# Optimization experiments

Measured on AMD Instinct MI355X. Metric: run time of the kernel, lower is better.

## Reference

```python
import jax, jax.numpy as jnp
import numpy as np

N = 20000      # total nodes (100 graphs x 200 nodes)
B = 100        # batch_size
PER = 200      # nodes per graph (uniform) -> max_num_nodes
E = 320000     # edges (before self-loops)
F_IN = 32      # num_features
HEADS = 10
OUT = 128      # output_dim
NEG_SLOPE = 0.2  # PyG GATConv default


def setup_inputs() -> dict:
    key = jax.random.key(0)
    ks = jax.random.split(key, 14)
    feats = jax.random.normal(ks[0], (N, F_IN), jnp.float32)
    src = jax.random.randint(ks[1], (E,), 0, N)
    dst = jax.random.randint(ks[2], (E,), 0, N)
    edge_index = jnp.stack([src, dst]).astype(jnp.int32)
    graph_id = jnp.repeat(jnp.arange(B, dtype=jnp.int32), PER)
    batch_num_nodes = jnp.full((B,), PER, jnp.int32)
    s1 = 1.0 / np.sqrt(F_IN)
    s2 = 1.0 / np.sqrt(F_IN * HEADS)
    s3 = 1.0 / np.sqrt(OUT)
    return {
        "feats": feats,
        "edge_index": edge_index,
        "graph_id": graph_id,
        "batch_num_nodes": batch_num_nodes,
        # GATConv 1: in F_IN -> HEADS x F_IN, concat
        "W1": jax.random.normal(ks[3], (F_IN, HEADS * F_IN), jnp.float32) * s1,
        "a1_src": jax.random.normal(ks[4], (HEADS, F_IN), jnp.float32) * s1,
        "a1_dst": jax.random.normal(ks[5], (HEADS, F_IN), jnp.float32) * s1,
        "b1": jnp.zeros((HEADS * F_IN,), jnp.float32),
        "W2": jax.random.normal(ks[6], (HEADS * F_IN, OUT), jnp.float32) * s2,
        "a2_src": jax.random.normal(ks[7], (1, OUT), jnp.float32) * s3,
        "a2_dst": jax.random.normal(ks[8], (1, OUT), jnp.float32) * s3,
        "b2": jnp.zeros((OUT,), jnp.float32),
        # shared fc_g1
        "fc_w": jax.random.normal(ks[9], (OUT, OUT), jnp.float32) * s3,
        "fc_b": jnp.zeros((OUT,), jnp.float32),
    }


def gat_conv(x, src, dst, W, a_src, a_dst, bias, heads, out_dim):
    # x: [N, Fin]; src/dst already include self-loops (PyG default add_self_loops=True)
    n = x.shape[0]
    xw = (x @ W).reshape(n, heads, out_dim)                 # [N,H,F]
    s_src = jnp.einsum('nhf,hf->nh', xw, a_src)             # [N,H]
    s_dst = jnp.einsum('nhf,hf->nh', xw, a_dst)
    e = jax.nn.leaky_relu(s_src[src] + s_dst[dst], NEG_SLOPE)  # [E,H]
    # segment softmax over incoming edges of each destination node
    m = jax.ops.segment_max(e, dst, num_segments=n)         # [N,H]
    ex = jnp.exp(e - m[dst])
    denom = jax.ops.segment_sum(ex, dst, num_segments=n)    # [N,H]
    alpha = ex / jnp.maximum(denom[dst], 1e-16)             # [E,H]
    out = jax.ops.segment_sum(alpha[:, :, None] * xw[src], dst, num_segments=n)  # [N,H,F]
    return out.reshape(n, heads * out_dim) + bias


def reference(feats, edge_index, graph_id, batch_num_nodes,
              W1, a1_src, a1_dst, b1, W2, a2_src, a2_dst, b2, fc_w, fc_b):
    n = feats.shape[0]
    loops = jnp.arange(n, dtype=edge_index.dtype)
    src = jnp.concatenate([edge_index[0], loops])
    dst = jnp.concatenate([edge_index[1], loops])
    x = feats.astype(jnp.float32)
    # dropout layers are identity in eval mode
    x = jax.nn.elu(gat_conv(x, src, dst, W1, a1_src, a1_dst, b1, HEADS, F_IN))
    x = gat_conv(x, src, dst, W2, a2_src, a2_dst, b2, 1, OUT)
    x = jax.nn.relu(x)                                       # [N, OUT]
    # dgl_split: scatter node feats into [B, max_num_nodes, OUT] padded tensor
    cum = jnp.concatenate([jnp.zeros((1,), jnp.int32),
                           jnp.cumsum(batch_num_nodes).astype(jnp.int32)])
    idx = jnp.arange(n, dtype=jnp.int32) - cum[graph_id] + graph_id * PER
    padded = jnp.zeros((B * PER, OUT), x.dtype).at[idx].set(x).reshape(B, PER, OUT)
    out = jax.nn.relu(padded @ fc_w + fc_b)                  # [B, PER, OUT]
    # global max pool per graph, then shared fc_g1 + relu
    pooled = jax.ops.segment_max(x, graph_id, num_segments=B)  # [B, OUT]
    pooled = jax.nn.relu(pooled @ fc_w + fc_b)
    return (out, pooled)
```

## Files before the change

### kernel.cpp

```cpp
#include <hip/hip_runtime.h>

#define N_NODES 20000
#define N_EDGES 320000
#define ETOT    (N_EDGES + N_NODES)
#define HEADS   10
#define F_IN    32
#define C1      (HEADS * F_IN)
#define C2      128
#define NB      100
#define PER     200
#define CAP     96
#define HSTRIDE 328
#define X2STRIDE 136

typedef __attribute__((ext_vector_type(8))) short bf16x8;
typedef __attribute__((ext_vector_type(4))) float floatx4;
typedef _Float16 f16;
typedef _Float16 f16x2 __attribute__((ext_vector_type(2)));
typedef _Float16 f16x4 __attribute__((ext_vector_type(4)));
typedef _Float16 f16x8 __attribute__((ext_vector_type(8)));

static __device__ __forceinline__ unsigned short f2bf(float f) {
    unsigned int u = __float_as_uint(f);
    unsigned int r = (u + 0x7fffu + ((u >> 16) & 1u)) >> 16;
    return (unsigned short)r;
}

#define SCAT_BLOCKS  ((ETOT + 255) / 256)
#define SCORE_BLOCKS ((N_NODES + 63) / 64)
#define W2P_BLOCKS   ((C1 * C2 + 255) / 256)
#define W1P_BLOCKS   ((HEADS * F_IN * F_IN + 255) / 256)
#define FCP_BLOCKS   ((C2 * C2 + 255) / 256)
#define F16_BLOCKS   ((N_NODES * F_IN / 4 + 255) / 256)
__global__ __launch_bounds__(256) void mega_prep_kernel(
        const int* __restrict__ ei, int* __restrict__ cursor, int* __restrict__ csr_src,
        const float* __restrict__ feats, f16* __restrict__ feats16,
        const float* __restrict__ W1, unsigned short* __restrict__ W1p,
        const float* __restrict__ W2, unsigned short* __restrict__ W2p,
        const float* __restrict__ fcw, f16* __restrict__ FCp,
        const float* __restrict__ a1s, const float* __restrict__ a1d,
        float* __restrict__ s_src, float* __restrict__ s_dst) {
    unsigned int b = blockIdx.x;
    if (b < SCAT_BLOCKS) {
        int e = b * 256 + threadIdx.x;
        if (e >= ETOT) return;
        int s, d;
        if (e < N_EDGES) { s = ei[e]; d = ei[N_EDGES + e]; }
        else             { s = e - N_EDGES; d = s; }
        int pos = atomicAdd(&cursor[d], 1);
        csr_src[(size_t)d * CAP + pos] = s;
        return;
    }
    b -= SCAT_BLOCKS;
    if (b < SCORE_BLOCKS) {
        __shared__ __align__(16) float A[64 * F_IN];
        __shared__ float Ws[C1], Wd[C1];
        int t = threadIdx.x;
        for (int o = t; o < C1; o += 256) {
            int k = o & 31, h = o >> 5;
            float ss = 0.f, dd = 0.f;
#pragma unroll
            for (int f = 0; f < F_IN; f++) {
                float wv = W1[k * C1 + h * 32 + f];
                ss += wv * a1s[h * 32 + f];
                dd += wv * a1d[h * 32 + f];
            }
            Ws[k * HEADS + h] = ss;
            Wd[k * HEADS + h] = dd;
        }
        int n0 = b * 64;
        int nrows = min(64, N_NODES - n0);
        const float4* fs = (const float4*)(feats + (size_t)n0 * F_IN);
        float4* Af = (float4*)A;
        for (int i = t; i < nrows * 8; i += 256) Af[i] = fs[i];
        __syncthreads();
        for (int o = t; o < nrows * HEADS; o += 256) {
            int nl = o / HEADS, h = o - nl * HEADS;
            const float* ar = A + nl * F_IN;
            float ss = 0.f, dd = 0.f;
#pragma unroll
            for (int k = 0; k < F_IN; k++) {
                float av = ar[k];
                ss += av * Ws[k * HEADS + h];
                dd += av * Wd[k * HEADS + h];
            }
            s_src[(size_t)(n0 + nl) * HEADS + h] = ss;
            s_dst[(size_t)(n0 + nl) * HEADS + h] = dd;
        }
        return;
    }
    b -= SCORE_BLOCKS;
    if (b < W2P_BLOCKS) {
        int o = b * 256 + threadIdx.x;
        if (o >= C1 * C2) return;
        int j    = o & 7;
        int lane = (o >> 3) & 63;
        int ct   = (o >> 9) & 7;
        int kb   = o >> 12;
        int k = kb * 32 + (lane >> 4) * 8 + j;
        int n = ct * 16 + (lane & 15);
        W2p[o] = f2bf(W2[k * C2 + n]);
        return;
    }
    b -= W2P_BLOCKS;
    if (b < W1P_BLOCKS) {
        int o = b * 256 + threadIdx.x;
        if (o >= HEADS * F_IN * F_IN) return;
        int j    = o & 7;
        int lane = (o >> 3) & 63;
        int ct   = (o >> 9) & 1;
        int h    = o >> 10;
        int k = (lane >> 4) * 8 + j;
        int f = ct * 16 + (lane & 15);
        W1p[o] = f2bf(W1[k * C1 + h * 32 + f]);
        return;
    }
    b -= W1P_BLOCKS;
    if (b < FCP_BLOCKS) {
        int o = b * 256 + threadIdx.x;
        if (o >= C2 * C2) return;
        int j    = o & 7;
        int lane = (o >> 3) & 63;
        int ct   = (o >> 9) & 7;
        int kb   = o >> 12;
        int k = kb * 32 + (lane >> 4) * 8 + j;
        int n = ct * 16 + (lane & 15);
        FCp[o] = (f16)fcw[k * C2 + n];
        return;
    }
    b -= FCP_BLOCKS;
    {
        int o = b * 256 + threadIdx.x;
        if (o < N_NODES * F_IN / 4) {
            float4 v = ((const float4*)feats)[o];
            f16* d = feats16 + 4 * o;
            d[0] = (f16)v.x; d[1] = (f16)v.y; d[2] = (f16)v.z; d[3] = (f16)v.w;
        }
    }
}

__global__ __launch_bounds__(512) void agg1h1g2_kernel(
        const f16* __restrict__ feats16, const float* __restrict__ s_src,
        const float* __restrict__ s_dst, const int* __restrict__ deg_arr,
        const int* __restrict__ csr_src,
        const unsigned short* __restrict__ W1p, const float* __restrict__ b1,
        const unsigned short* __restrict__ W2p,
        const float* __restrict__ a_src, const float* __restrict__ a_dst,
        f16* __restrict__ xw2h, float* __restrict__ s_src2, float* __restrict__ s_dst2) {
    union Smem {
        struct { f16 P[16][HEADS * 32]; int S[16][32]; } p1;
        unsigned short H[16 * HSTRIDE];
    };
    __shared__ __align__(16) Smem u;
    __shared__ __align__(16) unsigned short G[16 * HSTRIDE];
    __shared__ float redS[8][16], redD[8][16];

    int tid   = threadIdx.x;
    int wslot = tid >> 6;
    int lane  = tid & 63;
    int r     = tid >> 5;
    int l     = tid & 31;
    int row0  = blockIdx.x * 16;
    f16* P = u.p1.P[r];
    int* S = u.p1.S[r];
    const f16x2 ones = {(f16)1.f, (f16)1.f};
    const char* fb = (const char*)feats16 + 2 * l;

    {
        int n = row0 + r;
        int beg = n * CAP, deg = deg_arr[n];
        const float* sdp = s_dst + (size_t)n * HEADS;
        float sd[10];
#pragma unroll
        for (int q = 0; q < 5; q++) {
            float2 v = *(const float2*)(sdp + 2 * q);
            sd[2 * q] = v.x; sd[2 * q + 1] = v.y;
        }
        float g[10], la[10];
#pragma unroll
        for (int h = 0; h < 10; h++) { g[h] = 0.f; la[h] = 0.f; }

        for (int c0 = 0; c0 < deg; c0 += 32) {
            int dc = min(deg - c0, 32);
            bool act = l < dc;
            int s_e = csr_src[beg + c0 + min(l, dc - 1)];
            const float* ssp = s_src + (size_t)s_e * HEADS;
            float p[10];
#pragma unroll
            for (int q = 0; q < 5; q++) {
                float2 v = *(const float2*)(ssp + 2 * q);
                float e0 = v.x + sd[2 * q];
                float e1 = v.y + sd[2 * q + 1];
                e0 = (e0 >= 0.f) ? e0 : 0.2f * e0;
                e1 = (e1 >= 0.f) ? e1 : 0.2f * e1;
                p[2 * q]     = act ? __expf(e0) : 0.f;
                p[2 * q + 1] = act ? __expf(e1) : 0.f;
            }
            S[l] = s_e << 6;
#pragma unroll
            for (int h = 0; h < 10; h++) P[h * 32 + l] = (f16)p[h];
            asm volatile("s_waitcnt lgkmcnt(0)" ::: "memory");

            int dcp = (dc + 1) & ~1;
            for (int i = 0; i < dcp; i += 2) {
                int2 ss2 = *(const int2*)&S[i];
                f16x2 v;
                v.x = *(const f16*)(fb + ss2.x);
                v.y = *(const f16*)(fb + ss2.y);
#pragma unroll
                for (int h = 0; h < 10; h++) {
                    f16x2 pp = *(const f16x2*)&P[h * 32 + i];
                    g[h]  = __builtin_amdgcn_fdot2(pp, v, g[h], false);
                    la[h] = __builtin_amdgcn_fdot2(pp, ones, la[h], false);
                }
            }
            asm volatile("s_waitcnt lgkmcnt(0)" ::: "memory");
        }
        unsigned short* gr = &G[r * HSTRIDE + l];
#pragma unroll
        for (int h = 0; h < 10; h++)
            gr[h * 32] = f2bf(g[h] / fmaxf(la[h], 1e-16f));
    }
    __syncthreads();

    int quad = lane >> 4, col = lane & 15;
    for (int h = wslot; h < 10; h += 8) {
        bf16x8 a = *(const bf16x8*)&G[col * HSTRIDE + h * 32 + quad * 8];
        bf16x8 bA = ((const bf16x8*)W1p)[(h * 2 + 0) * 64 + lane];
        bf16x8 bB = ((const bf16x8*)W1p)[(h * 2 + 1) * 64 + lane];
        floatx4 z = {0.f, 0.f, 0.f, 0.f};
        floatx4 c0 = __builtin_amdgcn_mfma_f32_16x16x32_bf16(a, bA, z, 0, 0, 0);
        floatx4 c1 = __builtin_amdgcn_mfma_f32_16x16x32_bf16(a, bB, z, 0, 0, 0);
        float bias0 = b1[h * 32 + col];
        float bias1 = b1[h * 32 + 16 + col];
#pragma unroll
        for (int reg = 0; reg < 4; reg++) {
            int rr = quad * 4 + reg;
            float o0 = c0[reg] + bias0;
            float o1 = c1[reg] + bias1;
            o0 = (o0 > 0.f) ? o0 : (__expf(o0) - 1.f);
            o1 = (o1 > 0.f) ? o1 : (__expf(o1) - 1.f);
            u.H[rr * HSTRIDE + h * 32 + col]      = f2bf(o0);
            u.H[rr * HSTRIDE + h * 32 + 16 + col] = f2bf(o1);
        }
    }
    __syncthreads();

    floatx4 acc = {0.f, 0.f, 0.f, 0.f};
    const bf16x8* pb = (const bf16x8*)W2p;
#pragma unroll
    for (int kb = 0; kb < 10; kb++) {
        bf16x8 a = *(const bf16x8*)&u.H[col * HSTRIDE + kb * 32 + quad * 8];
        bf16x8 b = pb[(kb * 8 + wslot) * 64 + lane];
        acc = __builtin_amdgcn_mfma_f32_16x16x32_bf16(a, b, acc, 0, 0, 0);
    }
    float asv = a_src[wslot * 16 + col];
    float adv = a_dst[wslot * 16 + col];
#pragma unroll
    for (int reg = 0; reg < 4; reg++) {
        int row = row0 + quad * 4 + reg;
        float v = acc[reg];
        xw2h[(size_t)row * C2 + wslot * 16 + col] = (f16)v;
        float vs = v * asv, vd = v * adv;
#pragma unroll
        for (int off = 8; off >= 1; off >>= 1) {
            vs += __shfl_xor(vs, off);
            vd += __shfl_xor(vd, off);
        }
        if (col == 0) { redS[wslot][quad * 4 + reg] = vs; redD[wslot][quad * 4 + reg] = vd; }
    }
    __syncthreads();
    if (wslot == 0) {
        if (lane < 16) {
            float s = 0.f;
#pragma unroll
            for (int w2 = 0; w2 < 8; w2++) s += redS[w2][lane];
            s_src2[row0 + lane] = s;
        } else if (lane < 32) {
            int r2 = lane - 16;
            float d = 0.f;
#pragma unroll
            for (int w2 = 0; w2 < 8; w2++) d += redD[w2][r2];
            s_dst2[row0 + r2] = d;
        }
    }
}

__global__ __launch_bounds__(512) void agg2fc_kernel(
        const f16* __restrict__ xw2h, const float* __restrict__ s_src2,
        const float* __restrict__ s_dst2, const int* __restrict__ deg_arr,
        const int* __restrict__ csr_src, const float* __restrict__ b2,
        const f16* __restrict__ FCp, const float* __restrict__ fcb,
        float* __restrict__ out, int* __restrict__ pooledi) {
    __shared__ __align__(8) int2 shE[16][32];
    __shared__ __align__(16) f16 X[16 * X2STRIDE];
    int tid   = threadIdx.x;
    int wslot = tid >> 6;
    int lane  = tid & 63;
    int r     = tid >> 5;
    int l     = tid & 31;
    int row0  = blockIdx.x * 16;
    int2* E = shE[r];
    const char* xb = (const char*)xw2h + 8 * l;

    {
        int n = row0 + r;
        int beg = n * CAP, deg = deg_arr[n];
        float sd = s_dst2[n];
        float ldn = 0.f, a0 = 0.f, a1 = 0.f, a2 = 0.f, a3 = 0.f;

        for (int c0 = 0; c0 < deg; c0 += 32) {
            int dc = min(deg - c0, 32);
            bool act = l < dc;
            int s_e = csr_src[beg + c0 + min(l, dc - 1)];
            float e = s_src2[s_e] + sd;
            e = (e >= 0.f) ? e : 0.2f * e;
            float p = act ? __expf(e) : 0.f;
            float su = p;
#pragma unroll
            for (int off = 16; off >= 1; off >>= 1) su += __shfl_xor(su, off);
            ldn += su;

            E[l] = make_int2(s_e << 8, __float_as_int(p));
            asm volatile("s_waitcnt lgkmcnt(0)" ::: "memory");

            int dcr = (dc + 3) & ~3;
            for (int i = 0; i < dcr; i += 4) {
                int2 e0 = E[i + 0], e1 = E[i + 1], e2 = E[i + 2], e3 = E[i + 3];
                f16x4 v0 = *(const f16x4*)(xb + e0.x);
                f16x4 v1 = *(const f16x4*)(xb + e1.x);
                f16x4 v2 = *(const f16x4*)(xb + e2.x);
                f16x4 v3 = *(const f16x4*)(xb + e3.x);
                float p0 = __int_as_float(e0.y), p1 = __int_as_float(e1.y);
                float p2 = __int_as_float(e2.y), p3 = __int_as_float(e3.y);
                a0 += p0 * (float)v0[0] + p1 * (float)v1[0] + p2 * (float)v2[0] + p3 * (float)v3[0];
                a1 += p0 * (float)v0[1] + p1 * (float)v1[1] + p2 * (float)v2[1] + p3 * (float)v3[1];
                a2 += p0 * (float)v0[2] + p1 * (float)v1[2] + p2 * (float)v2[2] + p3 * (float)v3[2];
                a3 += p0 * (float)v0[3] + p1 * (float)v1[3] + p2 * (float)v2[3] + p3 * (float)v3[3];
            }
            asm volatile("s_waitcnt lgkmcnt(0)" ::: "memory");
        }

        float linv = 1.f / fmaxf(ldn, 1e-16f);
        float4 bb = *(const float4*)(b2 + 4 * l);
        f16x4 o;
        o[0] = (f16)fmaxf(a0 * linv + bb.x, 0.f);
        o[1] = (f16)fmaxf(a1 * linv + bb.y, 0.f);
        o[2] = (f16)fmaxf(a2 * linv + bb.z, 0.f);
        o[3] = (f16)fmaxf(a3 * linv + bb.w, 0.f);
        *(f16x4*)&X[r * X2STRIDE + 4 * l] = o;
    }
    __syncthreads();

    int quad = lane >> 4, col = lane & 15;
    floatx4 acc = {0.f, 0.f, 0.f, 0.f};
    const f16x8* pb = (const f16x8*)FCp;
#pragma unroll
    for (int kb = 0; kb < 4; kb++) {
        f16x8 a = *(const f16x8*)&X[col * X2STRIDE + kb * 32 + quad * 8];
        f16x8 b = pb[(kb * 8 + wslot) * 64 + lane];
        acc = __builtin_amdgcn_mfma_f32_16x16x32_f16(a, b, acc, 0, 0, 0);
    }
    float bias = fcb[wslot * 16 + col];
#pragma unroll
    for (int reg = 0; reg < 4; reg++) {
        int row = row0 + quad * 4 + reg;
        out[(size_t)row * C2 + wslot * 16 + col] = fmaxf(acc[reg] + bias, 0.f);
    }

    if (tid < C2) {
        int c = tid;
        int gA = row0 / PER;
        int gB = (row0 + 15) / PER;
        float mA = 0.f, mB = 0.f;
#pragma unroll
        for (int rr = 0; rr < 16; rr++) {
            float v = (float)X[rr * X2STRIDE + c];
            if ((row0 + rr) / PER == gA) mA = fmaxf(mA, v);
            else                         mB = fmaxf(mB, v);
        }
        atomicMax(&pooledi[gA * C2 + c], __float_as_int(mA));
        if (gB != gA) atomicMax(&pooledi[gB * C2 + c], __float_as_int(mB));
    }
}

__global__ void poolfc_kernel(const int* __restrict__ pooledi, const float* __restrict__ fcw,
                              const float* __restrict__ fcb, float* __restrict__ outp) {
    __shared__ float mx[C2];
    int g = blockIdx.x, t = threadIdx.x;
    mx[t] = __int_as_float(pooledi[g * C2 + t]);
    __syncthreads();
    float acc = 0.f;
    for (int k = 0; k < C2; k++) acc += mx[k] * fcw[k * C2 + t];
    outp[g * C2 + t] = fmaxf(acc + fcb[t], 0.f);
}

extern "C" void kernel_launch(void* const* d_in, const int* in_sizes, int n_in,
                              void* d_out, int out_size, void* d_ws, size_t ws_size,
                              hipStream_t stream) {
    const float* feats = (const float*)d_in[0];
    const int*   ei    = (const int*)d_in[1];
    const float* W1  = (const float*)d_in[4];
    const float* a1s = (const float*)d_in[5];
    const float* a1d = (const float*)d_in[6];
    const float* b1  = (const float*)d_in[7];
    const float* W2  = (const float*)d_in[8];
    const float* a2s = (const float*)d_in[9];
    const float* a2d = (const float*)d_in[10];
    const float* b2  = (const float*)d_in[11];
    const float* fcw = (const float*)d_in[12];
    const float* fcb = (const float*)d_in[13];

    float* out_main = (float*)d_out;
    float* out_pool = (float*)d_out + (size_t)N_NODES * C2;

    char* p = (char*)d_ws;
    auto alloc = [&](size_t bytes) {
        char* r = p;
        p += (bytes + 255) & ~(size_t)255;
        return r;
    };
    unsigned short* W2p  = (unsigned short*)alloc(sizeof(short) * C1 * C2);
    unsigned short* W1p  = (unsigned short*)alloc(sizeof(short) * HEADS * F_IN * F_IN);
    f16*   FCp     = (f16*)alloc(sizeof(f16) * C2 * C2);
    f16*   feats16 = (f16*)alloc(sizeof(f16) * (size_t)N_NODES * F_IN);
    f16*   xw2h    = (f16*)alloc(sizeof(f16) * (size_t)N_NODES * C2);
    float* s1s    = (float*)alloc(sizeof(float) * N_NODES * HEADS);
    float* s1d    = (float*)alloc(sizeof(float) * N_NODES * HEADS);
    float* s2s    = (float*)alloc(sizeof(float) * N_NODES);
    float* s2d    = (float*)alloc(sizeof(float) * N_NODES);
    const int NZ = N_NODES + NB * C2;
    int* zeros   = (int*)alloc(sizeof(int) * NZ);
    int* cursor  = zeros;
    int* pooledi = zeros + N_NODES;
    int* csr_src = (int*)alloc(sizeof(int) * N_NODES * CAP);

    hipMemsetAsync(zeros, 0, sizeof(int) * NZ, stream);

    mega_prep_kernel<<<SCAT_BLOCKS + SCORE_BLOCKS + W2P_BLOCKS + W1P_BLOCKS + FCP_BLOCKS + F16_BLOCKS,
                       256, 0, stream>>>(
        ei, cursor, csr_src, feats, feats16, W1, W1p, W2, W2p, fcw, FCp,
        a1s, a1d, s1s, s1d);

    agg1h1g2_kernel<<<1250, 512, 0, stream>>>(feats16, s1s, s1d, cursor, csr_src,
                                              W1p, b1, W2p, a2s, a2d, xw2h, s2s, s2d);
    agg2fc_kernel<<<1250, 512, 0, stream>>>(xw2h, s2s, s2d, cursor, csr_src, b2,
                                            FCp, fcb, out_main, pooledi);
    poolfc_kernel<<<NB, C2, 0, stream>>>(pooledi, fcw, fcb, out_pool);
}
```

Before: 157.9 us.

## Split layer-2 aggregation into two column-half passes and pad score rows

Layer-1 attention score arrays are padded to a 12-float stride so each row can be read with wider vector loads, and the layer-1 aggregation inner loop is unrolled by four edges. The layer-2 aggregation is split into two kernel launches, each gathering half of the 128 feature columns. The first pass writes its half to a new global buffer, and the second pass combines both halves for the FC MFMA. The split is meant to shrink the gather working set per pass so it fits better in cache, at the cost of recomputing the edge softmax in both passes plus an extra launch and a global round trip.

```diff
diff --git a/kernel.cpp b/kernel.cpp
--- a/kernel.cpp
+++ b/kernel.cpp
@@ -10,6 +10,7 @@
 #define NB      100
 #define PER     200
 #define CAP     96
+#define SSTRIDE 12
 #define HSTRIDE 328
 #define X2STRIDE 136
 
@@ -84,8 +85,8 @@
                 ss += av * Ws[k * HEADS + h];
                 dd += av * Wd[k * HEADS + h];
             }
-            s_src[(size_t)(n0 + nl) * HEADS + h] = ss;
-            s_dst[(size_t)(n0 + nl) * HEADS + h] = dd;
+            s_src[(size_t)(n0 + nl) * SSTRIDE + h] = ss;
+            s_dst[(size_t)(n0 + nl) * SSTRIDE + h] = dd;
         }
         return;
     }
@@ -169,12 +170,15 @@
     {
         int n = row0 + r;
         int beg = n * CAP, deg = deg_arr[n];
-        const float* sdp = s_dst + (size_t)n * HEADS;
+        const float* sdp = s_dst + (size_t)n * SSTRIDE;
         float sd[10];
-#pragma unroll
-        for (int q = 0; q < 5; q++) {
-            float2 v = *(const float2*)(sdp + 2 * q);
-            sd[2 * q] = v.x; sd[2 * q + 1] = v.y;
+        {
+            float4 v0 = *(const float4*)(sdp);
+            float4 v1 = *(const float4*)(sdp + 4);
+            float2 v2 = *(const float2*)(sdp + 8);
+            sd[0]=v0.x; sd[1]=v0.y; sd[2]=v0.z; sd[3]=v0.w;
+            sd[4]=v1.x; sd[5]=v1.y; sd[6]=v1.z; sd[7]=v1.w;
+            sd[8]=v2.x; sd[9]=v2.y;
         }
         float g[10], la[10];
 #pragma unroll
@@ -184,34 +188,45 @@
             int dc = min(deg - c0, 32);
             bool act = l < dc;
             int s_e = csr_src[beg + c0 + min(l, dc - 1)];
-            const float* ssp = s_src + (size_t)s_e * HEADS;
+            const float* ssp = s_src + (size_t)s_e * SSTRIDE;
+            float ss[10];
+            {
+                float4 v0 = *(const float4*)(ssp);
+                float4 v1 = *(const float4*)(ssp + 4);
+                float2 v2 = *(const float2*)(ssp + 8);
+                ss[0]=v0.x; ss[1]=v0.y; ss[2]=v0.z; ss[3]=v0.w;
+                ss[4]=v1.x; ss[5]=v1.y; ss[6]=v1.z; ss[7]=v1.w;
+                ss[8]=v2.x; ss[9]=v2.y;
+            }
             float p[10];
 #pragma unroll
-            for (int q = 0; q < 5; q++) {
-                float2 v = *(const float2*)(ssp + 2 * q);
-                float e0 = v.x + sd[2 * q];
-                float e1 = v.y + sd[2 * q + 1];
+            for (int h = 0; h < 10; h++) {
+                float e0 = ss[h] + sd[h];
                 e0 = (e0 >= 0.f) ? e0 : 0.2f * e0;
-                e1 = (e1 >= 0.f) ? e1 : 0.2f * e1;
-                p[2 * q]     = act ? __expf(e0) : 0.f;
-                p[2 * q + 1] = act ? __expf(e1) : 0.f;
+                p[h] = act ? __expf(e0) : 0.f;
             }
             S[l] = s_e << 6;
 #pragma unroll
             for (int h = 0; h < 10; h++) P[h * 32 + l] = (f16)p[h];
             asm volatile("s_waitcnt lgkmcnt(0)" ::: "memory");
 
-            int dcp = (dc + 1) & ~1;
-            for (int i = 0; i < dcp; i += 2) {
-                int2 ss2 = *(const int2*)&S[i];
-                f16x2 v;
-                v.x = *(const f16*)(fb + ss2.x);
-                v.y = *(const f16*)(fb + ss2.y);
+            int dcp = (dc + 3) & ~3;
+            for (int i = 0; i < dcp; i += 4) {
+                int4 ss4 = *(const int4*)&S[i];
+                f16x2 v01, v23;
+                v01.x = *(const f16*)(fb + ss4.x);
+                v01.y = *(const f16*)(fb + ss4.y);
+                v23.x = *(const f16*)(fb + ss4.z);
+                v23.y = *(const f16*)(fb + ss4.w);
 #pragma unroll
                 for (int h = 0; h < 10; h++) {
-                    f16x2 pp = *(const f16x2*)&P[h * 32 + i];
-                    g[h]  = __builtin_amdgcn_fdot2(pp, v, g[h], false);
-                    la[h] = __builtin_amdgcn_fdot2(pp, ones, la[h], false);
+                    f16x4 pp = *(const f16x4*)&P[h * 32 + i];
+                    f16x2 p01 = {pp[0], pp[1]};
+                    f16x2 p23 = {pp[2], pp[3]};
+                    g[h]  = __builtin_amdgcn_fdot2(p01, v01, g[h], false);
+                    g[h]  = __builtin_amdgcn_fdot2(p23, v23, g[h], false);
+                    la[h] = __builtin_amdgcn_fdot2(p01, ones, la[h], false);
+                    la[h] = __builtin_amdgcn_fdot2(p23, ones, la[h], false);
                 }
             }
             asm volatile("s_waitcnt lgkmcnt(0)" ::: "memory");
@@ -286,13 +301,15 @@
     }
 }
 
-__global__ __launch_bounds__(512) void agg2fc_kernel(
+template <int PASS>
+__global__ __launch_bounds__(512) void agg2pass_kernel(
         const f16* __restrict__ xw2h, const float* __restrict__ s_src2,
         const float* __restrict__ s_dst2, const int* __restrict__ deg_arr,
         const int* __restrict__ csr_src, const float* __restrict__ b2,
-        const f16* __restrict__ FCp, const float* __restrict__ fcb,
+        f16* __restrict__ Xh0, const f16* __restrict__ FCp,
+        const float* __restrict__ fcb,
         float* __restrict__ out, int* __restrict__ pooledi) {
-    __shared__ __align__(8) int2 shE[16][32];
+    __shared__ __align__(16) int2 shE[16][32];
     __shared__ __align__(16) f16 X[16 * X2STRIDE];
     int tid   = threadIdx.x;
     int wslot = tid >> 6;
@@ -301,13 +318,13 @@
     int l     = tid & 31;
     int row0  = blockIdx.x * 16;
     int2* E = shE[r];
-    const char* xb = (const char*)xw2h + 8 * l;
+    const char* xb = (const char*)xw2h + PASS * 128 + 4 * l;
 
     {
         int n = row0 + r;
         int beg = n * CAP, deg = deg_arr[n];
         float sd = s_dst2[n];
-        float ldn = 0.f, a0 = 0.f, a1 = 0.f, a2 = 0.f, a3 = 0.f;
+        float ldn = 0.f, a0 = 0.f, a1 = 0.f;
 
         for (int c0 = 0; c0 < deg; c0 += 32) {
             int dc = min(deg - c0, 32);
@@ -326,30 +343,34 @@
 
             int dcr = (dc + 3) & ~3;
             for (int i = 0; i < dcr; i += 4) {
-                int2 e0 = E[i + 0], e1 = E[i + 1], e2 = E[i + 2], e3 = E[i + 3];
-                f16x4 v0 = *(const f16x4*)(xb + e0.x);
-                f16x4 v1 = *(const f16x4*)(xb + e1.x);
-                f16x4 v2 = *(const f16x4*)(xb + e2.x);
-                f16x4 v3 = *(const f16x4*)(xb + e3.x);
-                float p0 = __int_as_float(e0.y), p1 = __int_as_float(e1.y);
-                float p2 = __int_as_float(e2.y), p3 = __int_as_float(e3.y);
-                a0 += p0 * (float)v0[0] + p1 * (float)v1[0] + p2 * (float)v2[0] + p3 * (float)v3[0];
-                a1 += p0 * (float)v0[1] + p1 * (float)v1[1] + p2 * (float)v2[1] + p3 * (float)v3[1];
-                a2 += p0 * (float)v0[2] + p1 * (float)v1[2] + p2 * (float)v2[2] + p3 * (float)v3[2];
-                a3 += p0 * (float)v0[3] + p1 * (float)v1[3] + p2 * (float)v2[3] + p3 * (float)v3[3];
+                int4 e01 = *(const int4*)&E[i];
+                int4 e23 = *(const int4*)&E[i + 2];
+                f16x2 v0 = *(const f16x2*)(xb + e01.x);
+                f16x2 v1 = *(const f16x2*)(xb + e01.z);
+                f16x2 v2 = *(const f16x2*)(xb + e23.x);
+                f16x2 v3 = *(const f16x2*)(xb + e23.z);
+                float p0 = __int_as_float(e01.y), p1 = __int_as_float(e01.w);
+                float p2 = __int_as_float(e23.y), p3 = __int_as_float(e23.w);
+                a0 += p0 * (float)v0.x + p1 * (float)v1.x + p2 * (float)v2.x + p3 * (float)v3.x;
+                a1 += p0 * (float)v0.y + p1 * (float)v1.y + p2 * (float)v2.y + p3 * (float)v3.y;
             }
             asm volatile("s_waitcnt lgkmcnt(0)" ::: "memory");
         }
 
         float linv = 1.f / fmaxf(ldn, 1e-16f);
-        float4 bb = *(const float4*)(b2 + 4 * l);
-        f16x4 o;
-        o[0] = (f16)fmaxf(a0 * linv + bb.x, 0.f);
-        o[1] = (f16)fmaxf(a1 * linv + bb.y, 0.f);
-        o[2] = (f16)fmaxf(a2 * linv + bb.z, 0.f);
-        o[3] = (f16)fmaxf(a3 * linv + bb.w, 0.f);
-        *(f16x4*)&X[r * X2STRIDE + 4 * l] = o;
-    }
+        float2 bb = *(const float2*)(b2 + PASS * 64 + 2 * l);
+        f16x2 o;
+        o.x = (f16)fmaxf(a0 * linv + bb.x, 0.f);
+        o.y = (f16)fmaxf(a1 * linv + bb.y, 0.f);
+        if (PASS == 0) {
+            *(f16x2*)&Xh0[(size_t)n * 64 + 2 * l] = o;
+        } else {
+            *(f16x2*)&X[r * X2STRIDE + 64 + 2 * l] = o;
+            *(f16x2*)&X[r * X2STRIDE + 2 * l] =
+                *(const f16x2*)&Xh0[(size_t)(row0 + r) * 64 + 2 * l];
+        }
+    }
+    if (PASS == 0) return;
     __syncthreads();
 
     int quad = lane >> 4, col = lane & 15;
@@ -425,8 +446,9 @@
     f16*   FCp     = (f16*)alloc(sizeof(f16) * C2 * C2);
     f16*   feats16 = (f16*)alloc(sizeof(f16) * (size_t)N_NODES * F_IN);
     f16*   xw2h    = (f16*)alloc(sizeof(f16) * (size_t)N_NODES * C2);
-    float* s1s    = (float*)alloc(sizeof(float) * N_NODES * HEADS);
-    float* s1d    = (float*)alloc(sizeof(float) * N_NODES * HEADS);
+    f16*   Xh0     = (f16*)alloc(sizeof(f16) * (size_t)N_NODES * 64);
+    float* s1s    = (float*)alloc(sizeof(float) * N_NODES * SSTRIDE);
+    float* s1d    = (float*)alloc(sizeof(float) * N_NODES * SSTRIDE);
     float* s2s    = (float*)alloc(sizeof(float) * N_NODES);
     float* s2d    = (float*)alloc(sizeof(float) * N_NODES);
     const int NZ = N_NODES + NB * C2;
@@ -444,7 +466,9 @@
 
     agg1h1g2_kernel<<<1250, 512, 0, stream>>>(feats16, s1s, s1d, cursor, csr_src,
                                               W1p, b1, W2p, a2s, a2d, xw2h, s2s, s2d);
-    agg2fc_kernel<<<1250, 512, 0, stream>>>(xw2h, s2s, s2d, cursor, csr_src, b2,
-                                            FCp, fcb, out_main, pooledi);
+    agg2pass_kernel<0><<<1250, 512, 0, stream>>>(xw2h, s2s, s2d, cursor, csr_src, b2,
+                                                 Xh0, FCp, fcb, out_main, pooledi);
+    agg2pass_kernel<1><<<1250, 512, 0, stream>>>(xw2h, s2s, s2d, cursor, csr_src, b2,
+                                                 Xh0, FCp, fcb, out_main, pooledi);
     poolfc_kernel<<<NB, C2, 0, stream>>>(pooledi, fcw, fcb, out_pool);
 }
```

After: 158.7 us. About the same (+0.5%).
